# Optimization experiments

Hardware: AMD Instinct MI355X
Metric: run time of the kernel (lower is better)

## Reference

```python
import jax, jax.numpy as jnp
import numpy as np

V = 78864; E = 300; H = 512; A = 300; T = 20; DEC_EMB = 512; START = 2


def _pos_encoding(n, d):
    pos = np.arange(n)[:, None].astype(np.float32)
    i = np.arange(d)[None, :]
    angle = pos / np.power(10000.0, (2 * (i // 2)).astype(np.float32) / d)
    pe = np.where(i % 2 == 0, np.sin(angle), np.cos(angle)).astype(np.float32)
    return jnp.asarray(pe)  # [n, d]


def _lstm_cell(x, h, c, Wih, Whh, b):
    g = x @ Wih.T + h @ Whh.T + b
    i, f, gg, o = jnp.split(g, 4, axis=-1)
    c = jax.nn.sigmoid(f) * c + jax.nn.sigmoid(i) * jnp.tanh(gg)
    h = jax.nn.sigmoid(o) * jnp.tanh(c)
    return h, c


def setup_inputs() -> dict:
    key = jax.random.key(0)
    ks = iter(jax.random.split(key, 48))
    B, L = 40, 1000
    def w(shape, s=0.02):
        return jax.random.normal(next(ks), shape, jnp.float32) * s
    def z(shape):
        return jnp.zeros(shape, jnp.float32)
    inp = dict(
        enc_in=jax.random.randint(next(ks), (B, L), 0, V),
        enc_out=jax.random.normal(next(ks), (B, L, H), jnp.float32),
        enc_mask=jnp.zeros((B, L), bool),
        inputs=jax.random.randint(next(ks), (B, T), 0, V),
        embed=w((V, E)),
        elmo1_Wih=w((4 * H, E)), elmo1_Whh=w((4 * H, H)), elmo1_b=z((4 * H,)),
        elmo2_Wih=w((4 * H, H)), elmo2_Whh=w((4 * H, H)), elmo2_b=z((4 * H,)),
        in_W=w((DEC_EMB, H + E + A + H)), in_b=z((DEC_EMB,)),
        rnn1_Wih=w((4 * H, DEC_EMB)), rnn1_Whh=w((4 * H, H)), rnn1_b=z((4 * H,)),
        att1_Wq=w((A, H)), att1_bq=z((A,)), att1_Wk=w((A, H)), att1_bk=z((A,)), att1_Wv=w((A, H)), att1_bv=z((A,)),
        rnn2_Wih=w((4 * H, A)), rnn2_Whh=w((4 * H, H)), rnn2_b=z((4 * H,)),
        att2_Wq=w((A, H)), att2_bq=z((A,)), att2_Wk=w((A, H)), att2_bk=z((A,)), att2_Wv=w((A, H)), att2_bv=z((A,)),
        copy_W=w((A, H)), copy_b=z((A,)),
        out_W=w((V, A)), out_b=z((V,)),
        scale=jnp.asarray(1.0, jnp.float32),
    )
    return inp


def _forward(enc_in, enc_out, enc_mask, inputs, embed,
             elmo1_Wih, elmo1_Whh, elmo1_b, elmo2_Wih, elmo2_Whh, elmo2_b,
             in_W, in_b, rnn1_Wih, rnn1_Whh, rnn1_b,
             att1_Wq, att1_bq, att1_Wk, att1_bk, att1_Wv, att1_bv,
             rnn2_Wih, rnn2_Whh, rnn2_b,
             att2_Wq, att2_bq, att2_Wk, att2_bk, att2_Wv, att2_bv,
             copy_W, copy_b, out_W, out_b, scale):
    B, L = enc_in.shape
    pe = _pos_encoding(T, DEC_EMB)  # [T, 512]
    # Precompute per-encoder projections (hoisted out of the step loop).
    K1 = jnp.einsum('blh,ah->bla', enc_out, att1_Wk) + att1_bk
    V1 = jnp.einsum('blh,ah->bla', enc_out, att1_Wv) + att1_bv
    K2 = jnp.einsum('blh,ah->bla', enc_out, att2_Wk) + att2_bk
    V2 = jnp.einsum('blh,ah->bla', enc_out, att2_Wv) + att2_bv
    copyK = jnp.tanh(jnp.einsum('blh,ah->bla', enc_out, copy_W) + copy_b)
    bidx = jnp.arange(B)[:, None]

    def attn(h, Wq, bq, K, Vp):
        q = h @ Wq.T + bq                          # [B, A]
        s = jnp.einsum('ba,bla->bl', q, K)
        s = jnp.where(enc_mask, -1e9, s)
        p = jax.nn.softmax(s, axis=-1)
        return jnp.einsum('bl,bla->ba', p, Vp)

    # teacher forcing with random_int=0 -> always use ground-truth inputs
    sym_in = jnp.concatenate([jnp.full((B, 1), START, inputs.dtype), inputs[:, :-1]], axis=1).T  # [T,B]
    sym_out = inputs.T  # [T,B]

    zf = lambda *s: jnp.zeros(s, enc_out.dtype)
    carry0 = (zf(B, H), zf(B, H), zf(B, H), zf(B, H),  # elmo h1,c1,h2,c2
              zf(B, H), zf(B, H), zf(B, H), zf(B, H),  # rnn1 h,c ; rnn2 h,c
              zf(B, A), zf(B, H))                       # dec_att_out, select_read

    def step(carry, xs):
        eh1, ec1, eh2, ec2, h1, c1, h2, c2, att, sel = carry
        pe_t, s_in, s_out = xs
        emb = embed[s_in]                                           # [B, E]
        eh1, ec1 = _lstm_cell(emb, eh1, ec1, elmo1_Wih, elmo1_Whh, elmo1_b)
        eh2, ec2 = _lstm_cell(eh1, eh2, ec2, elmo2_Wih, elmo2_Whh, elmo2_b)
        in_embed = jnp.concatenate([emb, eh2], axis=-1)              # [B, 812]
        dec_in = jnp.concatenate([in_embed, att, sel], axis=-1) @ in_W.T + in_b + pe_t
        h1, c1 = _lstm_cell(dec_in, h1, c1, rnn1_Wih, rnn1_Whh, rnn1_b)
        att = attn(h1, att1_Wq, att1_bq, K1, V1)
        h2, c2 = _lstm_cell(att, h2, c2, rnn2_Wih, rnn2_Whh, rnn2_b)
        att = attn(h2, att2_Wq, att2_bq, K2, V2) + att
        # copy scores
        s = jnp.einsum('ba,bla->bl', att, copyK)
        s = jnp.where(enc_mask, -1e9, s)
        score_c = jax.nn.softmax(s, axis=-1)
        score_e = score_c * scale * scale
        vocab = att @ out_W.T + out_b                                # [B, V]
        vocab = vocab.at[bidx, enc_in].add(score_e)
        sym_pred = jnp.argmax(vocab, axis=-1).astype(jnp.int32)
        eq = (enc_in == s_out[:, None]).astype(score_c.dtype)
        score_f = score_c * eq
        score_f = score_f / (jnp.sum(score_f, axis=-1, keepdims=True) + 1e-8)
        sel = jnp.einsum('bl,blh->bh', score_f, enc_out)
        return (eh1, ec1, eh2, ec2, h1, c1, h2, c2, att, sel), (vocab, sym_pred)

    _, (dec_out, syms) = jax.lax.scan(step, carry0, (pe, sym_in, sym_out))
    return jnp.transpose(dec_out, (1, 0, 2)), syms.T  # [B,T,V], [B,T]


def reference(enc_in, enc_out, enc_mask, inputs, embed,
              elmo1_Wih, elmo1_Whh, elmo1_b, elmo2_Wih, elmo2_Whh, elmo2_b,
              in_W, in_b, rnn1_Wih, rnn1_Whh, rnn1_b,
              att1_Wq, att1_bq, att1_Wk, att1_bk, att1_Wv, att1_bv,
              rnn2_Wih, rnn2_Whh, rnn2_b,
              att2_Wq, att2_bq, att2_Wk, att2_bk, att2_Wv, att2_bv,
              copy_W, copy_b, out_W, out_b, scale):
    return _forward(enc_in, enc_out, enc_mask, inputs, embed,
                    elmo1_Wih, elmo1_Whh, elmo1_b, elmo2_Wih, elmo2_Whh, elmo2_b,
                    in_W, in_b, rnn1_Wih, rnn1_Whh, rnn1_b,
                    att1_Wq, att1_bq, att1_Wk, att1_bk, att1_Wv, att1_bv,
                    rnn2_Wih, rnn2_Whh, rnn2_b,
                    att2_Wq, att2_bq, att2_Wk, att2_bk, att2_Wv, att2_bv,
                    copy_W, copy_b, out_W, out_b, scale)
```

## Files before the change

### kernel.cpp

```cpp
#include <hip/hip_runtime.h>
#include <math.h>

#define B_ 40
#define L_ 1000
#define H_ 512
#define A_ 300
#define T_ 20
#define E_ 300
#define V_ 78864
#define CIN_ 1624
#define START_ 2

__device__ __forceinline__ float sigm(float x){ return 1.0f/(1.0f+expf(-x)); }

__device__ __forceinline__ float waveMax(float v){
#pragma unroll
  for(int o=32;o>0;o>>=1) v=fmaxf(v,__shfl_down(v,o));
  return v;
}
__device__ __forceinline__ float waveSum(float v){
#pragma unroll
  for(int o=32;o>0;o>>=1) v+=__shfl_down(v,o);
  return v;
}

__global__ void k_pe(float* __restrict__ pe){
  int t=blockIdx.x, d=threadIdx.x;
  float ex=(float)(2*(d>>1))/512.0f;
  float ang=(float)t/powf(10000.0f,ex);
  pe[t*H_+d]=(d&1)?cosf(ang):sinf(ang);
}

__global__ __launch_bounds__(320) void k_copyk(const float* __restrict__ enc,
    const float* __restrict__ W, const float* __restrict__ bias, float* __restrict__ out){
  __shared__ float xs[H_];
  int row=blockIdx.x, tid=threadIdx.x;
  for(int k=tid;k<H_;k+=320) xs[k]=enc[(long)row*H_+k];
  __syncthreads();
  if(tid<A_){
    float acc=bias[tid];
    const float4* wr=(const float4*)(W+(long)tid*H_);
#pragma unroll 4
    for(int i=0;i<H_/4;i++){ float4 w=wr[i];
      acc+=xs[4*i]*w.x+xs[4*i+1]*w.y+xs[4*i+2]*w.z+xs[4*i+3]*w.w; }
    out[(long)row*A_+tid]=tanhf(acc);
  }
}

template<int XD, bool GATHER>
__global__ __launch_bounds__(256) void k_lstm(const float* __restrict__ xsrc,
    const int* __restrict__ inp, const float* __restrict__ embed, int t,
    const float* __restrict__ hr, const float* __restrict__ cr,
    float* __restrict__ hw, float* __restrict__ cw,
    const float* __restrict__ Wih, const float* __restrict__ Whh, const float* __restrict__ bias){
  __shared__ float xs[XD], hs[H_], g4[256];
  int b=blockIdx.y, hb=blockIdx.x, tid=threadIdx.x;
  const float* xr;
  if constexpr(GATHER){
    int si=(t==0)?START_:inp[b*T_+t-1];
    xr=embed+(long)si*XD;
  } else {
    xr=xsrc+(long)b*XD;
  }
  for(int k=tid;k<XD;k+=256) xs[k]=xr[k];
  for(int k=tid;k<H_;k+=256) hs[k]=hr[b*H_+k];
  __syncthreads();
  int gate=tid>>6, u=(hb<<6)+(tid&63), row=gate*H_+u;
  float acc=bias[row];
  const float4* wi=(const float4*)(Wih+(long)row*XD);
#pragma unroll 4
  for(int i=0;i<XD/4;i++){ float4 w=wi[i];
    acc+=xs[4*i]*w.x+xs[4*i+1]*w.y+xs[4*i+2]*w.z+xs[4*i+3]*w.w; }
  const float4* wh=(const float4*)(Whh+(long)row*H_);
#pragma unroll 4
  for(int i=0;i<H_/4;i++){ float4 w=wh[i];
    acc+=hs[4*i]*w.x+hs[4*i+1]*w.y+hs[4*i+2]*w.z+hs[4*i+3]*w.w; }
  g4[tid]=acc;
  __syncthreads();
  if(tid<64){
    int uu=(hb<<6)+tid;
    float gi=g4[tid],gf=g4[64+tid],gg=g4[128+tid],go=g4[192+tid];
    float c=cr[b*H_+uu];
    float cn=sigm(gf)*c+sigm(gi)*tanhf(gg);
    hw[b*H_+uu]=sigm(go)*tanhf(cn);
    cw[b*H_+uu]=cn;
  }
}

__global__ __launch_bounds__(256) void k_decin(const int* __restrict__ inp,
    const float* __restrict__ embed, int t,
    const float* __restrict__ eh2, const float* __restrict__ attprev,
    const float* __restrict__ selpart,
    const float* __restrict__ W, const float* __restrict__ bias,
    const float* __restrict__ pe, float* __restrict__ out){
  __shared__ float xs[CIN_];
  int b=blockIdx.y, tid=threadIdx.x;
  int si=(t==0)?START_:inp[b*T_+t-1];
  for(int k=tid;k<CIN_;k+=256){
    float v;
    if(k<E_) v=embed[(long)si*E_+k];
    else if(k<E_+H_) v=eh2[b*H_+k-E_];
    else if(k<E_+H_+A_) v=attprev[b*A_+k-(E_+H_)];
    else{
      int h=k-(E_+H_+A_);
      float s=0.f;
#pragma unroll
      for(int j=0;j<8;j++) s+=selpart[(b*8+j)*H_+h];
      v=s;
    }
    xs[k]=v;
  }
  __syncthreads();
  int d=blockIdx.x*256+tid;
  float acc=bias[d]+pe[t*H_+d];
  const float4* wr=(const float4*)(W+(long)d*CIN_);
#pragma unroll 2
  for(int i=0;i<CIN_/4;i++){ float4 w=wr[i];
    acc+=xs[4*i]*w.x+xs[4*i+1]*w.y+xs[4*i+2]*w.z+xs[4*i+3]*w.w; }
  out[b*H_+d]=acc;
}

__global__ __launch_bounds__(512) void k_q(const float* __restrict__ h,
    const float* __restrict__ Wq, const float* __restrict__ bq,
    const float* __restrict__ Wk, float* __restrict__ qk){
  __shared__ float hs[H_], qs[A_];
  int b=blockIdx.x, tid=threadIdx.x;
  hs[tid]=h[b*H_+tid];
  __syncthreads();
  if(tid<A_){
    float acc=bq[tid];
    const float4* wr=(const float4*)(Wq+(long)tid*H_);
#pragma unroll 4
    for(int i=0;i<H_/4;i++){ float4 w=wr[i];
      acc+=hs[4*i]*w.x+hs[4*i+1]*w.y+hs[4*i+2]*w.z+hs[4*i+3]*w.w; }
    qs[tid]=acc;
  }
  __syncthreads();
  float acc=0.f;
  for(int a=0;a<A_;a++) acc+=qs[a]*Wk[a*H_+tid];
  qk[b*H_+tid]=acc;
}

__global__ __launch_bounds__(128) void k_scores(const float* __restrict__ qk,
    const float* __restrict__ enc, const unsigned char* __restrict__ mask,
    float* __restrict__ s){
  __shared__ float qs[H_];
  int b=blockIdx.y, tid=threadIdx.x;
  for(int k=tid;k<H_;k+=128) qs[k]=qk[b*H_+k];
  __syncthreads();
  int l=blockIdx.x*128+tid;
  if(l<L_){
    float acc=0.f;
    const float4* er=(const float4*)(enc+((long)(b*L_+l))*H_);
#pragma unroll 4
    for(int i=0;i<H_/4;i++){ float4 e=er[i];
      acc+=qs[4*i]*e.x+qs[4*i+1]*e.y+qs[4*i+2]*e.z+qs[4*i+3]*e.w; }
    s[b*L_+l]=mask[b*L_+l]?-1e9f:acc;
  }
}

__global__ __launch_bounds__(512) void k_ctx(const float* __restrict__ s,
    const float* __restrict__ enc, float* __restrict__ part){
  __shared__ float e[L_];
  __shared__ float redm[8], reds[8];
  int b=blockIdx.y, j=blockIdx.x, tid=threadIdx.x;
  float lm=-3.0e38f;
  for(int l=tid;l<L_;l+=512){ float v=s[b*L_+l]; e[l]=v; lm=fmaxf(lm,v); }
  lm=waveMax(lm); if((tid&63)==0) redm[tid>>6]=lm;
  __syncthreads();
  float m=redm[0];
#pragma unroll
  for(int w2=1;w2<8;w2++) m=fmaxf(m,redm[w2]);
  float ls=0.f;
  for(int l=tid;l<L_;l+=512){ float ex=expf(e[l]-m); e[l]=ex; ls+=ex; }
  ls=waveSum(ls); if((tid&63)==0) reds[tid>>6]=ls;
  __syncthreads();
  float S=0.f;
#pragma unroll
  for(int w2=0;w2<8;w2++) S+=reds[w2];
  float inv=1.0f/S;
  float acc=0.f;
  int l0=j*125;
  for(int l=l0;l<l0+125;l++) acc+=e[l]*enc[((long)(b*L_+l))*H_+tid];
  part[(b*8+j)*H_+tid]=acc*inv;
}

template<bool ADD>
__global__ __launch_bounds__(512) void k_atto(const float* __restrict__ part,
    const float* __restrict__ Wv, const float* __restrict__ bv,
    const float* __restrict__ attprev, float* __restrict__ out){
  __shared__ float cs[H_];
  int b=blockIdx.x, tid=threadIdx.x;
  float c=0.f;
#pragma unroll
  for(int j=0;j<8;j++) c+=part[(b*8+j)*H_+tid];
  cs[tid]=c;
  __syncthreads();
  if(tid<A_){
    float acc=bv[tid];
    const float4* wr=(const float4*)(Wv+(long)tid*H_);
#pragma unroll 4
    for(int i=0;i<H_/4;i++){ float4 w=wr[i];
      acc+=cs[4*i]*w.x+cs[4*i+1]*w.y+cs[4*i+2]*w.z+cs[4*i+3]*w.w; }
    if constexpr(ADD) acc+=attprev[b*A_+tid];
    out[b*A_+tid]=acc;
  }
}

__global__ __launch_bounds__(128) void k_copysc(const float* __restrict__ att,
    const float* __restrict__ ck, const unsigned char* __restrict__ mask,
    float* __restrict__ s){
  __shared__ float as[A_];
  int b=blockIdx.y, tid=threadIdx.x;
  for(int k=tid;k<A_;k+=128) as[k]=att[b*A_+k];
  __syncthreads();
  int l=blockIdx.x*128+tid;
  if(l<L_){
    float acc=0.f;
    const float4* cr=(const float4*)(ck+((long)(b*L_+l))*A_);
#pragma unroll 5
    for(int i=0;i<A_/4;i++){ float4 c4=cr[i];
      acc+=as[4*i]*c4.x+as[4*i+1]*c4.y+as[4*i+2]*c4.z+as[4*i+3]*c4.w; }
    s[b*L_+l]=mask[b*L_+l]?-1e9f:acc;
  }
}

__global__ __launch_bounds__(256) void k_vocab(const float* __restrict__ att,
    const float* __restrict__ W, const float* __restrict__ bias, int t,
    float* __restrict__ dout){
  __shared__ float as[B_*A_];
  int tid=threadIdx.x;
  for(int k=tid;k<B_*A_;k+=256) as[k]=att[k];
  __syncthreads();
  int v=blockIdx.x*256+tid;
  if(v>=V_) return;
  float acc[B_];
#pragma unroll
  for(int b=0;b<B_;b++) acc[b]=0.f;
  const float4* wr=(const float4*)(W+(long)v*A_);
  for(int i=0;i<A_/4;i++){
    float4 w=wr[i];
    int a=4*i;
#pragma unroll
    for(int b=0;b<B_;b++){
      acc[b]+=as[b*A_+a]*w.x+as[b*A_+a+1]*w.y+as[b*A_+a+2]*w.z+as[b*A_+a+3]*w.w;
    }
  }
  float ob=bias[v];
#pragma unroll
  for(int b=0;b<B_;b++) dout[((long)(b*T_+t))*V_+v]=acc[b]+ob;
}

__global__ __launch_bounds__(128) void k_scatter(const float* __restrict__ s,
    const int* __restrict__ encin, const float* __restrict__ scale, int t,
    float* __restrict__ dout){
  __shared__ float row[L_];
  __shared__ float redm[2], reds[2];
  int b=blockIdx.y, tid=threadIdx.x;
  float lm=-3.0e38f;
  for(int l=tid;l<L_;l+=128){ float v=s[b*L_+l]; row[l]=v; lm=fmaxf(lm,v); }
  lm=waveMax(lm); if((tid&63)==0) redm[tid>>6]=lm;
  __syncthreads();
  float m=fmaxf(redm[0],redm[1]);
  float ls=0.f;
  for(int l=tid;l<L_;l+=128) ls+=expf(row[l]-m);
  ls=waveSum(ls); if((tid&63)==0) reds[tid>>6]=ls;
  __syncthreads();
  float S=reds[0]+reds[1];
  float f=scale[0]*scale[0]/S;
  int l=blockIdx.x*128+tid;
  if(l<L_){
    float p=expf(row[l]-m)*f;
    atomicAdd(dout+((long)(b*T_+t))*V_+encin[b*L_+l],p);
  }
}

__global__ __launch_bounds__(256) void k_argmax(int t, float* __restrict__ dout){
  __shared__ float vs[256];
  __shared__ int is[256];
  int b=blockIdx.x, tid=threadIdx.x;
  const float* row=dout+((long)(b*T_+t))*V_;
  float best=-3.0e38f; int bi=0;
  for(int v=tid;v<V_;v+=256){ float x=row[v]; if(x>best){best=x;bi=v;} }
  vs[tid]=best; is[tid]=bi;
  __syncthreads();
  for(int off=128;off>0;off>>=1){
    if(tid<off){
      float ov=vs[tid+off]; int oi=is[tid+off];
      if(ov>vs[tid]||(ov==vs[tid]&&oi<is[tid])){ vs[tid]=ov; is[tid]=oi; }
    }
    __syncthreads();
  }
  if(tid==0) dout[(long)B_*T_*V_+b*T_+t]=(float)is[0];
}

__global__ __launch_bounds__(512) void k_sel(const float* __restrict__ s,
    const int* __restrict__ encin, const int* __restrict__ inp, int t,
    const float* __restrict__ enc, float* __restrict__ part){
  __shared__ float e[L_];
  __shared__ float redm[8], reds[8], redq[8];
  int b=blockIdx.y, j=blockIdx.x, tid=threadIdx.x;
  int so=inp[b*T_+t];
  float lm=-3.0e38f;
  for(int l=tid;l<L_;l+=512){ float v=s[b*L_+l]; e[l]=v; lm=fmaxf(lm,v); }
  lm=waveMax(lm); if((tid&63)==0) redm[tid>>6]=lm;
  __syncthreads();
  float m=redm[0];
#pragma unroll
  for(int w2=1;w2<8;w2++) m=fmaxf(m,redm[w2]);
  float ls=0.f, lq=0.f;
  for(int l=tid;l<L_;l+=512){
    float ex=expf(e[l]-m);
    float pe_=(encin[b*L_+l]==so)?ex:0.f;
    e[l]=pe_; ls+=ex; lq+=pe_;
  }
  ls=waveSum(ls); lq=waveSum(lq);
  if((tid&63)==0){ reds[tid>>6]=ls; redq[tid>>6]=lq; }
  __syncthreads();
  float S=0.f,Q=0.f;
#pragma unroll
  for(int w2=0;w2<8;w2++){ S+=reds[w2]; Q+=redq[w2]; }
  float inv=1.0f/(Q+1e-8f*S);
  float acc=0.f;
  int l0=j*125;
  for(int l=l0;l<l0+125;l++) acc+=e[l]*enc[((long)(b*L_+l))*H_+tid];
  part[(b*8+j)*H_+tid]=acc*inv;
}

extern "C" void kernel_launch(void* const* d_in, const int* in_sizes, int n_in,
                              void* d_out, int out_size, void* d_ws, size_t ws_size,
                              hipStream_t stream){
  const int* enc_in=(const int*)d_in[0];
  const float* enc_out=(const float*)d_in[1];
  const unsigned char* enc_mask=(const unsigned char*)d_in[2];
  const int* inputs=(const int*)d_in[3];
  const float* embed=(const float*)d_in[4];
  const float* e1Wih=(const float*)d_in[5], *e1Whh=(const float*)d_in[6], *e1b=(const float*)d_in[7];
  const float* e2Wih=(const float*)d_in[8], *e2Whh=(const float*)d_in[9], *e2b=(const float*)d_in[10];
  const float* inW=(const float*)d_in[11], *inb=(const float*)d_in[12];
  const float* r1Wih=(const float*)d_in[13], *r1Whh=(const float*)d_in[14], *r1b=(const float*)d_in[15];
  const float* a1Wq=(const float*)d_in[16], *a1bq=(const float*)d_in[17];
  const float* a1Wk=(const float*)d_in[18];
  const float* a1Wv=(const float*)d_in[20], *a1bv=(const float*)d_in[21];
  const float* r2Wih=(const float*)d_in[22], *r2Whh=(const float*)d_in[23], *r2b=(const float*)d_in[24];
  const float* a2Wq=(const float*)d_in[25], *a2bq=(const float*)d_in[26];
  const float* a2Wk=(const float*)d_in[27];
  const float* a2Wv=(const float*)d_in[29], *a2bv=(const float*)d_in[30];
  const float* cW=(const float*)d_in[31], *cb=(const float*)d_in[32];
  const float* oW=(const float*)d_in[33], *ob=(const float*)d_in[34];
  const float* scale=(const float*)d_in[35];
  float* dout=(float*)d_out;
  float* w=(float*)d_ws;

  size_t off=0;
  float* copyK=w+off; off+=(size_t)B_*L_*A_;
  float* pe=w+off;    off+=T_*H_;
  float* st=w+off;    off+=16*B_*H_;
  float* att1=w+off;  off+=B_*A_;
  float* att2=w+off;  off+=B_*A_;
  float* qk=w+off;    off+=B_*H_;
  float* s1=w+off;    off+=B_*L_;
  float* scc=w+off;   off+=B_*L_;
  float* ctxp=w+off;  off+=B_*8*H_;
  float* selp=w+off;  off+=B_*8*H_;
  float* decin=w+off; off+=B_*H_;

  hipMemsetAsync(pe,0,(off-(size_t)B_*L_*A_)*sizeof(float),stream);
  k_pe<<<T_,H_,0,stream>>>(pe);
  k_copyk<<<B_*L_,320,0,stream>>>(enc_out,cW,cb,copyK);

  auto S=[&](int i){ return st+(size_t)i*(B_*H_); };
  for(int t=0;t<T_;t++){
    int rp=t&1, wp=rp^1;
    float *eh1r=S(0+rp),*eh1w=S(0+wp),*ec1r=S(2+rp),*ec1w=S(2+wp);
    float *eh2r=S(4+rp),*eh2w=S(4+wp),*ec2r=S(6+rp),*ec2w=S(6+wp);
    float *h1r=S(8+rp),*h1w=S(8+wp),*c1r=S(10+rp),*c1w=S(10+wp);
    float *h2r=S(12+rp),*h2w=S(12+wp),*c2r=S(14+rp),*c2w=S(14+wp);

    k_lstm<E_,true><<<dim3(8,B_),256,0,stream>>>(nullptr,inputs,embed,t,eh1r,ec1r,eh1w,ec1w,e1Wih,e1Whh,e1b);
    k_lstm<H_,false><<<dim3(8,B_),256,0,stream>>>(eh1w,nullptr,nullptr,t,eh2r,ec2r,eh2w,ec2w,e2Wih,e2Whh,e2b);
    k_decin<<<dim3(2,B_),256,0,stream>>>(inputs,embed,t,eh2w,att2,selp,inW,inb,pe,decin);
    k_lstm<H_,false><<<dim3(8,B_),256,0,stream>>>(decin,nullptr,nullptr,t,h1r,c1r,h1w,c1w,r1Wih,r1Whh,r1b);
    k_q<<<B_,512,0,stream>>>(h1w,a1Wq,a1bq,a1Wk,qk);
    k_scores<<<dim3(8,B_),128,0,stream>>>(qk,enc_out,enc_mask,s1);
    k_ctx<<<dim3(8,B_),512,0,stream>>>(s1,enc_out,ctxp);
    k_atto<false><<<B_,512,0,stream>>>(ctxp,a1Wv,a1bv,nullptr,att1);
    k_lstm<A_,false><<<dim3(8,B_),256,0,stream>>>(att1,nullptr,nullptr,t,h2r,c2r,h2w,c2w,r2Wih,r2Whh,r2b);
    k_q<<<B_,512,0,stream>>>(h2w,a2Wq,a2bq,a2Wk,qk);
    k_scores<<<dim3(8,B_),128,0,stream>>>(qk,enc_out,enc_mask,s1);
    k_ctx<<<dim3(8,B_),512,0,stream>>>(s1,enc_out,ctxp);
    k_atto<true><<<B_,512,0,stream>>>(ctxp,a2Wv,a2bv,att1,att2);
    k_copysc<<<dim3(8,B_),128,0,stream>>>(att2,copyK,enc_mask,scc);
    k_vocab<<<(V_+255)/256,256,0,stream>>>(att2,oW,ob,t,dout);
    k_scatter<<<dim3(8,B_),128,0,stream>>>(scc,enc_in,scale,t,dout);
    k_argmax<<<B_,256,0,stream>>>(t,dout);
    k_sel<<<dim3(8,B_),512,0,stream>>>(scc,enc_in,inputs,t,enc_out,selp);
  }
}
```

Before: 18.73 ms.

## Rework vocab, copy-key, score and LSTM kernels; fuse scatter with selection

Several kernels are restructured at once. The vocab projection now stages W tiles in shared memory and reads a transposed attention vector from global memory instead of staging all of att in LDS. The copy-key projection has each thread compute 16 encoder rows so weight loads are reused. The score kernels switch to wave-per-row coalesced reductions, the LSTM kernels read x and h straight from global memory, and the scatter and selection kernels are merged into one. The aim is better memory coalescing and occupancy plus fewer launches, at the cost of more global reads in some kernels and an extra transposed buffer.

```diff
diff --git a/kernel.cpp b/kernel.cpp
--- a/kernel.cpp
+++ b/kernel.cpp
@@ -23,6 +23,11 @@
   for(int o=32;o>0;o>>=1) v+=__shfl_down(v,o);
   return v;
 }
+__device__ __forceinline__ float waveSumXor(float v){
+#pragma unroll
+  for(int o=32;o>0;o>>=1) v+=__shfl_xor(v,o);
+  return v;
+}
 
 __global__ void k_pe(float* __restrict__ pe){
   int t=blockIdx.x, d=threadIdx.x;
@@ -33,18 +38,24 @@
 
 __global__ __launch_bounds__(320) void k_copyk(const float* __restrict__ enc,
     const float* __restrict__ W, const float* __restrict__ bias, float* __restrict__ out){
-  __shared__ float xs[H_];
-  int row=blockIdx.x, tid=threadIdx.x;
-  for(int k=tid;k<H_;k+=320) xs[k]=enc[(long)row*H_+k];
-  __syncthreads();
-  if(tid<A_){
-    float acc=bias[tid];
-    const float4* wr=(const float4*)(W+(long)tid*H_);
-#pragma unroll 4
-    for(int i=0;i<H_/4;i++){ float4 w=wr[i];
-      acc+=xs[4*i]*w.x+xs[4*i+1]*w.y+xs[4*i+2]*w.z+xs[4*i+3]*w.w; }
-    out[(long)row*A_+tid]=tanhf(acc);
-  }
+  int b=blockIdx.y, l0=blockIdx.x*16, a=threadIdx.x;
+  if(a>=A_) return;
+  int lcnt=min(16,L_-l0);
+  float acc[16];
+  float bv=bias[a];
+#pragma unroll
+  for(int l=0;l<16;l++) acc[l]=bv;
+  const float4* wr=(const float4*)(W+(long)a*H_);
+  for(int i=0;i<H_/4;i++){
+    float4 w=wr[i];
+#pragma unroll
+    for(int l=0;l<16;l++){
+      int row=b*L_+min(l0+l,L_-1);
+      float4 x=((const float4*)enc)[(long)row*(H_/4)+i];
+      acc[l]+=x.x*w.x+x.y*w.y+x.z*w.z+x.w*w.w;
+    }
+  }
+  for(int l=0;l<lcnt;l++) out[((long)(b*L_+l0+l))*A_+a]=tanhf(acc[l]);
 }
 
 template<int XD, bool GATHER>
@@ -53,28 +64,26 @@
     const float* __restrict__ hr, const float* __restrict__ cr,
     float* __restrict__ hw, float* __restrict__ cw,
     const float* __restrict__ Wih, const float* __restrict__ Whh, const float* __restrict__ bias){
-  __shared__ float xs[XD], hs[H_], g4[256];
+  __shared__ float g4[256];
   int b=blockIdx.y, hb=blockIdx.x, tid=threadIdx.x;
-  const float* xr;
+  const float4* xr4;
   if constexpr(GATHER){
     int si=(t==0)?START_:inp[b*T_+t-1];
-    xr=embed+(long)si*XD;
+    xr4=(const float4*)(embed+(long)si*XD);
   } else {
-    xr=xsrc+(long)b*XD;
-  }
-  for(int k=tid;k<XD;k+=256) xs[k]=xr[k];
-  for(int k=tid;k<H_;k+=256) hs[k]=hr[b*H_+k];
-  __syncthreads();
+    xr4=(const float4*)(xsrc+(long)b*XD);
+  }
+  const float4* hr4=(const float4*)(hr+(long)b*H_);
   int gate=tid>>6, u=(hb<<6)+(tid&63), row=gate*H_+u;
   float acc=bias[row];
   const float4* wi=(const float4*)(Wih+(long)row*XD);
 #pragma unroll 4
-  for(int i=0;i<XD/4;i++){ float4 w=wi[i];
-    acc+=xs[4*i]*w.x+xs[4*i+1]*w.y+xs[4*i+2]*w.z+xs[4*i+3]*w.w; }
+  for(int i=0;i<XD/4;i++){ float4 w=wi[i]; float4 x=xr4[i];
+    acc+=x.x*w.x+x.y*w.y+x.z*w.z+x.w*w.w; }
   const float4* wh=(const float4*)(Whh+(long)row*H_);
 #pragma unroll 4
-  for(int i=0;i<H_/4;i++){ float4 w=wh[i];
-    acc+=hs[4*i]*w.x+hs[4*i+1]*w.y+hs[4*i+2]*w.z+hs[4*i+3]*w.w; }
+  for(int i=0;i<H_/4;i++){ float4 w=wh[i]; float4 h4=hr4[i];
+    acc+=h4.x*w.x+h4.y*w.y+h4.z*w.z+h4.w*w.w; }
   g4[tid]=acc;
   __syncthreads();
   if(tid<64){
@@ -141,21 +150,26 @@
   qk[b*H_+tid]=acc;
 }
 
-__global__ __launch_bounds__(128) void k_scores(const float* __restrict__ qk,
+__global__ __launch_bounds__(256) void k_scores(const float* __restrict__ qk,
     const float* __restrict__ enc, const unsigned char* __restrict__ mask,
     float* __restrict__ s){
   __shared__ float qs[H_];
-  int b=blockIdx.y, tid=threadIdx.x;
-  for(int k=tid;k<H_;k+=128) qs[k]=qk[b*H_+k];
-  __syncthreads();
-  int l=blockIdx.x*128+tid;
-  if(l<L_){
-    float acc=0.f;
+  int b=blockIdx.y, j=blockIdx.x, tid=threadIdx.x;
+  qs[tid]=qk[b*H_+tid]; qs[tid+256]=qk[b*H_+tid+256];
+  __syncthreads();
+  int wv=tid>>6, lane=tid&63;
+  const float4* qs4=(const float4*)qs;
+  for(int i=0;i<32;i++){
+    int idx=i*4+wv;
+    if(idx>=125) break;
+    int l=j*125+idx;
     const float4* er=(const float4*)(enc+((long)(b*L_+l))*H_);
-#pragma unroll 4
-    for(int i=0;i<H_/4;i++){ float4 e=er[i];
-      acc+=qs[4*i]*e.x+qs[4*i+1]*e.y+qs[4*i+2]*e.z+qs[4*i+3]*e.w; }
-    s[b*L_+l]=mask[b*L_+l]?-1e9f:acc;
+    float4 q1=qs4[lane], e1=er[lane];
+    float p=q1.x*e1.x+q1.y*e1.y+q1.z*e1.z+q1.w*e1.w;
+    float4 q2=qs4[64+lane], e2=er[64+lane];
+    p+=q2.x*e2.x+q2.y*e2.y+q2.z*e2.z+q2.w*e2.w;
+    p=waveSumXor(p);
+    if(lane==0) s[b*L_+l]=mask[b*L_+l]?-1e9f:p;
   }
 }
 
@@ -188,7 +202,7 @@
 template<bool ADD>
 __global__ __launch_bounds__(512) void k_atto(const float* __restrict__ part,
     const float* __restrict__ Wv, const float* __restrict__ bv,
-    const float* __restrict__ attprev, float* __restrict__ out){
+    const float* __restrict__ attprev, float* __restrict__ out, float* __restrict__ outT){
   __shared__ float cs[H_];
   int b=blockIdx.x, tid=threadIdx.x;
   float c=0.f;
@@ -204,75 +218,118 @@
       acc+=cs[4*i]*w.x+cs[4*i+1]*w.y+cs[4*i+2]*w.z+cs[4*i+3]*w.w; }
     if constexpr(ADD) acc+=attprev[b*A_+tid];
     out[b*A_+tid]=acc;
-  }
-}
-
-__global__ __launch_bounds__(128) void k_copysc(const float* __restrict__ att,
+    if constexpr(ADD) outT[tid*B_+b]=acc;
+  }
+}
+
+__global__ __launch_bounds__(256) void k_copysc(const float* __restrict__ att,
     const float* __restrict__ ck, const unsigned char* __restrict__ mask,
     float* __restrict__ s){
   __shared__ float as[A_];
-  int b=blockIdx.y, tid=threadIdx.x;
-  for(int k=tid;k<A_;k+=128) as[k]=att[b*A_+k];
-  __syncthreads();
-  int l=blockIdx.x*128+tid;
-  if(l<L_){
-    float acc=0.f;
-    const float4* cr=(const float4*)(ck+((long)(b*L_+l))*A_);
-#pragma unroll 5
-    for(int i=0;i<A_/4;i++){ float4 c4=cr[i];
-      acc+=as[4*i]*c4.x+as[4*i+1]*c4.y+as[4*i+2]*c4.z+as[4*i+3]*c4.w; }
-    s[b*L_+l]=mask[b*L_+l]?-1e9f:acc;
-  }
-}
-
-__global__ __launch_bounds__(256) void k_vocab(const float* __restrict__ att,
+  int b=blockIdx.y, j=blockIdx.x, tid=threadIdx.x;
+  for(int k=tid;k<A_;k+=256) as[k]=att[b*A_+k];
+  __syncthreads();
+  int wv=tid>>6, lane=tid&63;
+  for(int i=0;i<32;i++){
+    int idx=i*4+wv;
+    if(idx>=125) break;
+    int l=j*125+idx;
+    const float* cr=ck+((long)(b*L_+l))*A_;
+    float p=0.f;
+#pragma unroll
+    for(int it=0;it<4;it++){ int k=it*64+lane; p+=as[k]*cr[k]; }
+    { int k=256+lane; if(k<A_) p+=as[k]*cr[k]; }
+    p=waveSumXor(p);
+    if(lane==0) s[b*L_+l]=mask[b*L_+l]?-1e9f:p;
+  }
+}
+
+__global__ __launch_bounds__(256) void k_vocab(const float* __restrict__ attT,
     const float* __restrict__ W, const float* __restrict__ bias, int t,
     float* __restrict__ dout){
-  __shared__ float as[B_*A_];
+  __shared__ float wt[256*33];
   int tid=threadIdx.x;
-  for(int k=tid;k<B_*A_;k+=256) as[k]=att[k];
-  __syncthreads();
   int v=blockIdx.x*256+tid;
-  if(v>=V_) return;
+  bool ok=v<V_;
+  int v0=blockIdx.x*256;
   float acc[B_];
 #pragma unroll
   for(int b=0;b<B_;b++) acc[b]=0.f;
-  const float4* wr=(const float4*)(W+(long)v*A_);
-  for(int i=0;i<A_/4;i++){
-    float4 w=wr[i];
-    int a=4*i;
-#pragma unroll
-    for(int b=0;b<B_;b++){
-      acc[b]+=as[b*A_+a]*w.x+as[b*A_+a+1]*w.y+as[b*A_+a+2]*w.z+as[b*A_+a+3]*w.w;
+  for(int c=0;c<10;c++){
+    int a0=c*32;
+    int aw=(c<9)?32:12;
+    __syncthreads();
+    if(c<9){
+      for(int idx=tid;idx<256*32;idx+=256){
+        int vr=idx>>5, ar=idx&31;
+        float val=(v0+vr<V_)?W[(long)(v0+vr)*A_+a0+ar]:0.f;
+        wt[vr*33+ar]=val;
+      }
+    } else {
+      for(int idx=tid;idx<256*12;idx+=256){
+        int vr=idx/12, ar=idx-vr*12;
+        float val=(v0+vr<V_)?W[(long)(v0+vr)*A_+a0+ar]:0.f;
+        wt[vr*33+ar]=val;
+      }
     }
-  }
-  float ob=bias[v];
-#pragma unroll
-  for(int b=0;b<B_;b++) dout[((long)(b*T_+t))*V_+v]=acc[b]+ob;
-}
-
-__global__ __launch_bounds__(128) void k_scatter(const float* __restrict__ s,
-    const int* __restrict__ encin, const float* __restrict__ scale, int t,
+    __syncthreads();
+    for(int a=0;a<aw;a++){
+      float wv=wt[tid*33+a];
+      const float4* at4=(const float4*)(attT+(long)(a0+a)*B_);
+#pragma unroll
+      for(int bq=0;bq<10;bq++){
+        float4 t4=at4[bq];
+        acc[4*bq+0]+=wv*t4.x; acc[4*bq+1]+=wv*t4.y;
+        acc[4*bq+2]+=wv*t4.z; acc[4*bq+3]+=wv*t4.w;
+      }
+    }
+  }
+  if(ok){
+    float ob=bias[v];
+#pragma unroll
+    for(int b=0;b<B_;b++) dout[((long)(b*T_+t))*V_+v]=acc[b]+ob;
+  }
+}
+
+__global__ __launch_bounds__(512) void k_scatsel(const float* __restrict__ s,
+    const int* __restrict__ encin, const int* __restrict__ inp,
+    const float* __restrict__ scale, int t,
+    const float* __restrict__ enc, float* __restrict__ part,
     float* __restrict__ dout){
-  __shared__ float row[L_];
-  __shared__ float redm[2], reds[2];
-  int b=blockIdx.y, tid=threadIdx.x;
+  __shared__ float e[L_], e2[L_];
+  __shared__ float redm[8], reds[8], redq[8];
+  int b=blockIdx.y, j=blockIdx.x, tid=threadIdx.x;
+  int so=inp[b*T_+t];
   float lm=-3.0e38f;
-  for(int l=tid;l<L_;l+=128){ float v=s[b*L_+l]; row[l]=v; lm=fmaxf(lm,v); }
+  for(int l=tid;l<L_;l+=512){ float v=s[b*L_+l]; e[l]=v; lm=fmaxf(lm,v); }
   lm=waveMax(lm); if((tid&63)==0) redm[tid>>6]=lm;
   __syncthreads();
-  float m=fmaxf(redm[0],redm[1]);
-  float ls=0.f;
-  for(int l=tid;l<L_;l+=128) ls+=expf(row[l]-m);
-  ls=waveSum(ls); if((tid&63)==0) reds[tid>>6]=ls;
-  __syncthreads();
-  float S=reds[0]+reds[1];
-  float f=scale[0]*scale[0]/S;
-  int l=blockIdx.x*128+tid;
-  if(l<L_){
-    float p=expf(row[l]-m)*f;
+  float m=redm[0];
+#pragma unroll
+  for(int w2=1;w2<8;w2++) m=fmaxf(m,redm[w2]);
+  float ls=0.f, lq=0.f;
+  for(int l=tid;l<L_;l+=512){
+    float ex=expf(e[l]-m);
+    float pe_=(encin[b*L_+l]==so)?ex:0.f;
+    e[l]=ex; e2[l]=pe_; ls+=ex; lq+=pe_;
+  }
+  ls=waveSum(ls); lq=waveSum(lq);
+  if((tid&63)==0){ reds[tid>>6]=ls; redq[tid>>6]=lq; }
+  __syncthreads();
+  float S=0.f,Q=0.f;
+#pragma unroll
+  for(int w2=0;w2<8;w2++){ S+=reds[w2]; Q+=redq[w2]; }
+  int l0=j*125;
+  if(tid<125){
+    int l=l0+tid;
+    float f=scale[0]*scale[0]/S;
+    float p=e[l]*f;
     atomicAdd(dout+((long)(b*T_+t))*V_+encin[b*L_+l],p);
   }
+  float inv=1.0f/(Q+1e-8f*S);
+  float acc=0.f;
+  for(int l=l0;l<l0+125;l++) acc+=e2[l]*enc[((long)(b*L_+l))*H_+tid];
+  part[(b*8+j)*H_+tid]=acc*inv;
 }
 
 __global__ __launch_bounds__(256) void k_argmax(int t, float* __restrict__ dout){
@@ -292,39 +349,6 @@
     __syncthreads();
   }
   if(tid==0) dout[(long)B_*T_*V_+b*T_+t]=(float)is[0];
-}
-
-__global__ __launch_bounds__(512) void k_sel(const float* __restrict__ s,
-    const int* __restrict__ encin, const int* __restrict__ inp, int t,
-    const float* __restrict__ enc, float* __restrict__ part){
-  __shared__ float e[L_];
-  __shared__ float redm[8], reds[8], redq[8];
-  int b=blockIdx.y, j=blockIdx.x, tid=threadIdx.x;
-  int so=inp[b*T_+t];
-  float lm=-3.0e38f;
-  for(int l=tid;l<L_;l+=512){ float v=s[b*L_+l]; e[l]=v; lm=fmaxf(lm,v); }
-  lm=waveMax(lm); if((tid&63)==0) redm[tid>>6]=lm;
-  __syncthreads();
-  float m=redm[0];
-#pragma unroll
-  for(int w2=1;w2<8;w2++) m=fmaxf(m,redm[w2]);
-  float ls=0.f, lq=0.f;
-  for(int l=tid;l<L_;l+=512){
-    float ex=expf(e[l]-m);
-    float pe_=(encin[b*L_+l]==so)?ex:0.f;
-    e[l]=pe_; ls+=ex; lq+=pe_;
-  }
-  ls=waveSum(ls); lq=waveSum(lq);
-  if((tid&63)==0){ reds[tid>>6]=ls; redq[tid>>6]=lq; }
-  __syncthreads();
-  float S=0.f,Q=0.f;
-#pragma unroll
-  for(int w2=0;w2<8;w2++){ S+=reds[w2]; Q+=redq[w2]; }
-  float inv=1.0f/(Q+1e-8f*S);
-  float acc=0.f;
-  int l0=j*125;
-  for(int l=l0;l<l0+125;l++) acc+=e[l]*enc[((long)(b*L_+l))*H_+tid];
-  part[(b*8+j)*H_+tid]=acc*inv;
 }
 
 extern "C" void kernel_launch(void* const* d_in, const int* in_sizes, int n_in,
@@ -358,6 +382,7 @@
   float* st=w+off;    off+=16*B_*H_;
   float* att1=w+off;  off+=B_*A_;
   float* att2=w+off;  off+=B_*A_;
+  float* attT=w+off;  off+=A_*B_;
   float* qk=w+off;    off+=B_*H_;
   float* s1=w+off;    off+=B_*L_;
   float* scc=w+off;   off+=B_*L_;
@@ -367,7 +392,7 @@
 
   hipMemsetAsync(pe,0,(off-(size_t)B_*L_*A_)*sizeof(float),stream);
   k_pe<<<T_,H_,0,stream>>>(pe);
-  k_copyk<<<B_*L_,320,0,stream>>>(enc_out,cW,cb,copyK);
+  k_copyk<<<dim3((L_+15)/16,B_),320,0,stream>>>(enc_out,cW,cb,copyK);
 
   auto S=[&](int i){ return st+(size_t)i*(B_*H_); };
   for(int t=0;t<T_;t++){
@@ -382,18 +407,17 @@
     k_decin<<<dim3(2,B_),256,0,stream>>>(inputs,embed,t,eh2w,att2,selp,inW,inb,pe,decin);
     k_lstm<H_,false><<<dim3(8,B_),256,0,stream>>>(decin,nullptr,nullptr,t,h1r,c1r,h1w,c1w,r1Wih,r1Whh,r1b);
     k_q<<<B_,512,0,stream>>>(h1w,a1Wq,a1bq,a1Wk,qk);
-    k_scores<<<dim3(8,B_),128,0,stream>>>(qk,enc_out,enc_mask,s1);
+    k_scores<<<dim3(8,B_),256,0,stream>>>(qk,enc_out,enc_mask,s1);
     k_ctx<<<dim3(8,B_),512,0,stream>>>(s1,enc_out,ctxp);
-    k_atto<false><<<B_,512,0,stream>>>(ctxp,a1Wv,a1bv,nullptr,att1);
+    k_atto<false><<<B_,512,0,stream>>>(ctxp,a1Wv,a1bv,nullptr,att1,nullptr);
     k_lstm<A_,false><<<dim3(8,B_),256,0,stream>>>(att1,nullptr,nullptr,t,h2r,c2r,h2w,c2w,r2Wih,r2Whh,r2b);
     k_q<<<B_,512,0,stream>>>(h2w,a2Wq,a2bq,a2Wk,qk);
-    k_scores<<<dim3(8,B_),128,0,stream>>>(qk,enc_out,enc_mask,s1);
+    k_scores<<<dim3(8,B_),256,0,stream>>>(qk,enc_out,enc_mask,s1);
     k_ctx<<<dim3(8,B_),512,0,stream>>>(s1,enc_out,ctxp);
-    k_atto<true><<<B_,512,0,stream>>>(ctxp,a2Wv,a2bv,att1,att2);
-    k_copysc<<<dim3(8,B_),128,0,stream>>>(att2,copyK,enc_mask,scc);
-    k_vocab<<<(V_+255)/256,256,0,stream>>>(att2,oW,ob,t,dout);
-    k_scatter<<<dim3(8,B_),128,0,stream>>>(scc,enc_in,scale,t,dout);
+    k_atto<true><<<B_,512,0,stream>>>(ctxp,a2Wv,a2bv,att1,att2,attT);
+    k_copysc<<<dim3(8,B_),256,0,stream>>>(att2,copyK,enc_mask,scc);
+    k_vocab<<<(V_+255)/256,256,0,stream>>>(attT,oW,ob,t,dout);
+    k_scatsel<<<dim3(8,B_),512,0,stream>>>(scc,enc_in,inputs,scale,t,enc_out,selp,dout);
     k_argmax<<<B_,256,0,stream>>>(t,dout);
-    k_sel<<<dim3(8,B_),512,0,stream>>>(scc,enc_in,inputs,t,enc_out,selp);
-  }
-}
+  }
+}
```

New measurement: 18.39 ms. Within noise of the previous version (-1.8%).
